# Performance work log

Measured on AMD Instinct MI355X. Metric: run time of the kernel, lower is better.

The kernel has to match this reference:

```python
import jax, jax.numpy as jnp
import numpy as np

B, S, D, H = 4, 2048, 768, 12


def setup_inputs() -> dict:
    key = jax.random.key(0)
    k1, k2, k3, k4 = jax.random.split(key, 4)
    std = D ** (-0.5)
    x = jax.random.normal(k1, (B, S, D), dtype=jnp.float32)
    W_QKV = jax.random.normal(k2, (3, D, D), dtype=jnp.float32) * std
    W_O = jax.random.normal(k3, (D, D), dtype=jnp.float32) * std
    token_positions = jnp.sort(jax.random.randint(k4, (B, S), 0, S), axis=-1).astype(jnp.int64)
    return {"x": x, "W_QKV": W_QKV, "W_O": W_O, "token_positions": token_positions,
            "num_heads": H, "theta": 10000}


def _apply_rope(t, cos, sin):
    # t: (B, H, S, Hd); cos/sin: (B, 1, S, Hd/2). Interleaved even/odd pairs.
    te, to = t[..., 0::2], t[..., 1::2]
    re = te * cos - to * sin
    ro = te * sin + to * cos
    return jnp.stack([re, ro], axis=-1).reshape(t.shape)


def reference(x, W_QKV, W_O, token_positions, num_heads, theta):
    b, s, d = x.shape
    hd = d // num_heads  # d_head = d_k = d_v
    # fused QKV projection: Q = x @ W_QKV[0].T etc.
    qkv = jnp.einsum('bsd,kod->kbso', x, W_QKV)              # (3, B, S, D)
    qkv = qkv.reshape(3, b, s, num_heads, hd).transpose(0, 1, 3, 2, 4)  # (3, B, H, S, Hd)
    q, k, v = qkv[0], qkv[1], qkv[2]
    # RoPE angles: pos * theta^(-2j/d_k)
    inv_freq = jnp.asarray(theta, x.dtype) ** (-(jnp.arange(0, hd, 2, dtype=x.dtype) / hd))
    angles = token_positions.astype(x.dtype)[..., None] * inv_freq    # (B, S, Hd/2)
    cos = jnp.cos(angles)[:, None]                                     # (B, 1, S, Hd/2)
    sin = jnp.sin(angles)[:, None]
    q = _apply_rope(q, cos, sin)
    k = _apply_rope(k, cos, sin)
    # causal attention
    scores = jnp.einsum('bhqd,bhkd->bhqk', q, k) / (hd ** 0.5)        # (B, H, S, S)
    causal = jnp.tril(jnp.ones((s, s), dtype=bool))
    scores = jnp.where(causal, scores, -jnp.inf)
    probs = jax.nn.softmax(scores, axis=-1)
    out = jnp.einsum('bhqk,bhkd->bhqd', probs, v)                      # (B, H, S, Hd)
    out = out.transpose(0, 2, 1, 3).reshape(b, s, d)
    return out @ W_O.T
```

## Files before the change

kernel.cpp:

```cpp
#include <hip/hip_runtime.h>
#include <hip/hip_bf16.h>

typedef __bf16 bf16;
typedef __bf16 bf16x8 __attribute__((ext_vector_type(8)));
typedef __bf16 bf16x4 __attribute__((ext_vector_type(4)));
typedef short  s16x4  __attribute__((ext_vector_type(4)));
typedef float  f32x4  __attribute__((ext_vector_type(4)));

#if defined(__has_builtin)
#if __has_builtin(__builtin_amdgcn_mfma_f32_16x16x16bf16_1k)
#define HAVE_MFMA16 1
#endif
#if __has_builtin(__builtin_amdgcn_exp2f)
#define EXP2(x) __builtin_amdgcn_exp2f(x)
#else
#define EXP2(x) exp2f(x)
#endif
#else
#define EXP2(x) exp2f(x)
#endif

__device__ __forceinline__ void gl_lds16(const void* g, void* l) {
  __builtin_amdgcn_global_load_lds(
      (__attribute__((address_space(1))) const void*)g,
      (__attribute__((address_space(3))) void*)l, 16, 0, 0);
}

__device__ __forceinline__ f32x4 mfma32(bf16x8 a, bf16x8 b, f32x4 c) {
  return __builtin_amdgcn_mfma_f32_16x16x32_bf16(a, b, c, 0, 0, 0);
}
#if HAVE_MFMA16
__device__ __forceinline__ f32x4 mfma16(s16x4 a, s16x4 b, f32x4 c) {
  return __builtin_amdgcn_mfma_f32_16x16x16bf16_1k(a, b, c, 0, 0, 0);
}
#endif

__global__ void prep(const float* __restrict__ a, bf16* __restrict__ da,
                     const float* __restrict__ b, bf16* __restrict__ db,
                     const float* __restrict__ c, bf16* __restrict__ dc,
                     const int* __restrict__ tpos, const int* __restrict__ thetap,
                     float2* __restrict__ tab) {
  int bx = blockIdx.x;
  if (bx >= 8448) {
    int i = (bx - 8448) * 256 + threadIdx.x;
    int d2 = i & 31;
    int bs = i >> 5;
    float lt = log2f((float)(*thetap));
    float fr = exp2f(-(float)d2 * (1.0f / 32.0f) * lt);
    float ang = (float)tpos[bs] * fr;
    float sn, cs;
    sincosf(ang, &sn, &cs);
    tab[i] = make_float2(cs, sn);
    return;
  }
  const float* s; bf16* d; int i;
  if (bx < 6144)      { s = a; d = da; i = bx * 256 + threadIdx.x; }
  else if (bx < 7872) { s = b; d = db; i = (bx - 6144) * 256 + threadIdx.x; }
  else                { s = c; d = dc; i = (bx - 7872) * 256 + threadIdx.x; }
  float4 v = ((const float4*)s)[i];
  bf16x4 o;
  o[0] = (bf16)v.x; o[1] = (bf16)v.y; o[2] = (bf16)v.z; o[3] = (bf16)v.w;
  ((bf16x4*)d)[i] = o;
}

template <int MODE>
__global__ void gemm_bt(const bf16* __restrict__ A, const bf16* __restrict__ Bm,
                        void* __restrict__ Cout, bf16* __restrict__ Vout,
                        const float2* __restrict__ tab) {
  constexpr int K = 768;
  __shared__ __align__(16) char As[2][128 * 64];
  __shared__ __align__(16) char Bs[2][128 * 64];
  const int tid = threadIdx.x;
  const int w = tid >> 6, lane = tid & 63;
  const int quad = lane >> 4, l15 = lane & 15;
  const int wrow = w >> 1, wcol = w & 1;
  const int m0 = blockIdx.x * 128, n0 = blockIdx.y * 128;

  f32x4 acc[4][4];
#pragma unroll
  for (int mt = 0; mt < 4; ++mt)
#pragma unroll
    for (int nt = 0; nt < 4; ++nt) acc[mt][nt] = (f32x4){0.f, 0.f, 0.f, 0.f};

  auto stage = [&](int k0, int bufi) {
#pragma unroll
    for (int i = 0; i < 2; ++i) {
      int L = i * 256 + tid;
      int r = L >> 2, cl = L & 3;
      int cg = cl ^ ((r >> 1) & 3);
      gl_lds16(A + (size_t)(m0 + r) * K + k0 + cg * 8, As[bufi] + (i * 256 + w * 64) * 16);
      gl_lds16(Bm + (size_t)(n0 + r) * K + k0 + cg * 8, Bs[bufi] + (i * 256 + w * 64) * 16);
    }
  };

  stage(0, 0);
  int buf = 0;

  for (int k0 = 0; k0 < K; k0 += 32) {
    __syncthreads();
    if (k0 + 32 < K) stage(k0 + 32, buf ^ 1);
    const char* Ab = As[buf];
    const char* Bb = Bs[buf];

    bf16x8 af[4], bfr[4];
#pragma unroll
    for (int mt = 0; mt < 4; ++mt) {
      int r = wrow * 64 + mt * 16 + l15;
      int cl = quad ^ ((r >> 1) & 3);
      af[mt] = *(const bf16x8*)(Ab + r * 64 + cl * 16);
    }
#pragma unroll
    for (int nt = 0; nt < 4; ++nt) {
      int r = wcol * 64 + nt * 16 + l15;
      int cl = quad ^ ((r >> 1) & 3);
      bfr[nt] = *(const bf16x8*)(Bb + r * 64 + cl * 16);
    }
#pragma unroll
    for (int mt = 0; mt < 4; ++mt)
#pragma unroll
      for (int nt = 0; nt < 4; ++nt)
        acc[mt][nt] = mfma32(af[mt], bfr[nt], acc[mt][nt]);
    buf ^= 1;
  }

#pragma unroll
  for (int mt = 0; mt < 4; ++mt)
#pragma unroll
    for (int nt = 0; nt < 4; ++nt)
#pragma unroll
      for (int r = 0; r < 4; ++r) {
        int m = m0 + wrow * 64 + mt * 16 + quad * 4 + r;
        int n = n0 + wcol * 64 + nt * 16 + l15;
        float v = acc[mt][nt][r];
        if (MODE == 0) {
          ((float*)Cout)[(size_t)m * 768 + n] = v;
        } else {
          int mat = n / 768, rem = n % 768;
          int hh = rem >> 6, d = rem & 63;
          int bb = m >> 11, s = m & 2047;
          if (mat == 2) {
            Vout[(((size_t)(bb * 12 + hh) * 64 + d) * 2048) + s] = (bf16)v;
          } else {
            float partner = __shfl_xor(v, 1);
            float2 t = tab[((size_t)m << 5) + ((rem >> 1) & 31)];
            float out = v * t.x + ((n & 1) ? partner : -partner) * t.y;
            if (mat == 0) out *= 0.18033688011112042f;
            ((bf16*)Cout)[(((size_t)(mat * 4 + bb) * 12 + hh) * 2048 + s) * 64 + d] = (bf16)out;
          }
        }
      }
}

__global__ __launch_bounds__(256, 4)
void attn(const bf16* __restrict__ qkv, const bf16* __restrict__ vt,
          bf16* __restrict__ aout) {
  const int bx = blockIdx.x;
  const int qt = 15 - (bx / 48);
  const int bh = bx % 48;
  const int b = bh / 12, h = bh % 12;
  const int tid = threadIdx.x, w = tid >> 6, lane = tid & 63;
  const int quad = lane >> 4, l15 = lane & 15;
  const bf16* Q  = qkv + (size_t)bh * (2048 * 64);
  const bf16* Kp = qkv + (size_t)(48 + bh) * (2048 * 64);
  const bf16* Vt = vt + (size_t)bh * (64 * 2048);
  __shared__ __align__(16) char Ks[2][64 * 128];
  __shared__ __align__(16) char Vs[2][64 * 128];

  const int qbase = qt * 128 + w * 32;
  const int kmax = qbase >> 6;
  bf16x8 qf[2][2];
#pragma unroll
  for (int j = 0; j < 2; ++j) {
    qf[j][0] = *(const bf16x8*)(Q + (size_t)(qbase + j * 16 + l15) * 64 + quad * 8);
    qf[j][1] = *(const bf16x8*)(Q + (size_t)(qbase + j * 16 + l15) * 64 + 32 + quad * 8);
  }

  float li[2] = {0.f, 0.f};
  f32x4 o[2][4];
#pragma unroll
  for (int j = 0; j < 2; ++j)
#pragma unroll
    for (int dt = 0; dt < 4; ++dt) o[j][dt] = (f32x4){0.f, 0.f, 0.f, 0.f};

  auto stage = [&](int kb, int bufi) {
#pragma unroll
    for (int i = 0; i < 2; ++i) {
      int L = i * 256 + tid;
      int r = L >> 3, cl = L & 7, cg = cl ^ (r & 7);
      gl_lds16(Kp + (size_t)(kb * 64 + r) * 64 + cg * 8, Ks[bufi] + L * 16);
      gl_lds16(Vt + (size_t)r * 2048 + kb * 64 + cg * 8, Vs[bufi] + L * 16);
    }
  };

  stage(0, 0);
  int buf = 0;
  const int nkt = 2 * qt + 2;

  for (int kb = 0; kb < nkt; ++kb) {
    __syncthreads();
    if (kb + 1 < nkt) stage(kb + 1, buf ^ 1);
    if (kb <= kmax) {
      const char* Kb = Ks[buf];
      const char* Vb = Vs[buf];

      float S[2][16];
      __builtin_amdgcn_s_setprio(1);
#pragma unroll
      for (int sk = 0; sk < 4; ++sk) {
        int r = sk * 16 + l15;
        int cl0 = quad ^ (r & 7);
        int cl1 = (4 + quad) ^ (r & 7);
        bf16x8 kf0 = *(const bf16x8*)(Kb + r * 128 + cl0 * 16);
        bf16x8 kf1 = *(const bf16x8*)(Kb + r * 128 + cl1 * 16);
#pragma unroll
        for (int j = 0; j < 2; ++j) {
          f32x4 st = (f32x4){0.f, 0.f, 0.f, 0.f};
          st = mfma32(kf0, qf[j][0], st);
          st = mfma32(kf1, qf[j][1], st);
#pragma unroll
          for (int rr = 0; rr < 4; ++rr) S[j][sk * 4 + rr] = st[rr];
        }
      }
      __builtin_amdgcn_s_setprio(0);
      if (kb == kmax) {
#pragma unroll
        for (int j = 0; j < 2; ++j)
#pragma unroll
          for (int sk = 0; sk < 4; ++sk)
#pragma unroll
            for (int rr = 0; rr < 4; ++rr) {
              int key = kb * 64 + sk * 16 + quad * 4 + rr;
              if (key > qbase + j * 16 + l15) S[j][sk * 4 + rr] = -1e30f;
            }
      }

#if HAVE_MFMA16
      s16x4 pf[2][4];
#endif
#pragma unroll
      for (int j = 0; j < 2; ++j) {
        float rs = 0.f;
#pragma unroll
        for (int sk = 0; sk < 4; ++sk) {
          bf16x4 pb;
#pragma unroll
          for (int rr = 0; rr < 4; ++rr) {
            float p = EXP2(S[j][sk * 4 + rr]);
            rs += p;
            pb[rr] = (bf16)p;
#if !HAVE_MFMA16
            S[j][sk * 4 + rr] = p;
#endif
          }
#if HAVE_MFMA16
          pf[j][sk] = __builtin_bit_cast(s16x4, pb);
#else
          (void)pb;
#endif
        }
        rs += __shfl_xor(rs, 16);
        rs += __shfl_xor(rs, 32);
        li[j] += rs;
      }

#if HAVE_MFMA16
      __builtin_amdgcn_s_setprio(1);
#pragma unroll
      for (int sk = 0; sk < 4; ++sk)
#pragma unroll
        for (int dt = 0; dt < 4; ++dt) {
          int rr = dt * 16 + l15;
          int c = sk * 2 + (quad >> 1);
          int cl = c ^ (rr & 7);
          s16x4 vf = *(const s16x4*)(Vb + rr * 128 + cl * 16 + (quad & 1) * 8);
          o[0][dt] = mfma16(pf[0][sk], vf, o[0][dt]);
          o[1][dt] = mfma16(pf[1][sk], vf, o[1][dt]);
        }
      __builtin_amdgcn_s_setprio(0);
#else
#pragma unroll
      for (int j = 0; j < 2; ++j)
#pragma unroll
        for (int kc = 0; kc < 2; ++kc) {
          bf16x8 af;
#pragma unroll
          for (int jj = 0; jj < 8; ++jj) {
            int sq = (quad & 1) * 2 + (jj >> 2);
            int src = sq * 16 + l15;
            float v0 = __shfl(S[j][kc * 8 + (jj & 3)], src);
            float v1 = __shfl(S[j][kc * 8 + 4 + (jj & 3)], src);
            af[jj] = (bf16)((quad < 2) ? v0 : v1);
          }
#pragma unroll
          for (int dt = 0; dt < 4; ++dt) {
            int rr = dt * 16 + l15;
            int c = kc * 4 + quad;
            int cl = c ^ (rr & 7);
            bf16x8 vf = *(const bf16x8*)(Vb + rr * 128 + cl * 16);
            o[j][dt] = mfma32(af, vf, o[j][dt]);
          }
        }
#endif
    }
    buf ^= 1;
  }

#pragma unroll
  for (int j = 0; j < 2; ++j) {
    float lr[4];
#pragma unroll
    for (int rr = 0; rr < 4; ++rr)
      lr[rr] = __builtin_amdgcn_rcpf(__shfl(li[j], quad * 4 + rr));
#pragma unroll
    for (int dt = 0; dt < 4; ++dt)
#pragma unroll
      for (int rr = 0; rr < 4; ++rr) {
        int q = qbase + j * 16 + quad * 4 + rr;
        int n = h * 64 + dt * 16 + l15;
        aout[((size_t)b * 2048 + q) * 768 + n] = (bf16)(o[j][dt][rr] * lr[rr]);
      }
  }
}

extern "C" void kernel_launch(void* const* d_in, const int* in_sizes, int n_in,
                              void* d_out, int out_size, void* d_ws, size_t ws_size,
                              hipStream_t stream) {
  const float* x    = (const float*)d_in[0];
  const float* wqkv = (const float*)d_in[1];
  const float* wo   = (const float*)d_in[2];
  const int* tpos   = (const int*)d_in[3];
  const int* thetap = (const int*)d_in[5];

  char* ws = (char*)d_ws;
  bf16* xb    = (bf16*)(ws);
  bf16* wqkvb = (bf16*)(ws + 12582912);
  bf16* wob   = (bf16*)(ws + 16121856);
  bf16* qkv   = (bf16*)(ws + 17301504);
  bf16* vtb   = (bf16*)(ws + 55050240);
  float2* tab = (float2*)(ws + 42467328);

  prep<<<9472, 256, 0, stream>>>(x, xb, wqkv, wqkvb, wo, wob, tpos, thetap, tab);
  gemm_bt<1><<<dim3(64, 18), 256, 0, stream>>>(xb, wqkvb, (void*)qkv, vtb, tab);
  attn<<<768, 256, 0, stream>>>(qkv, vtb, xb);
  gemm_bt<0><<<dim3(64, 6), 256, 0, stream>>>(xb, wob, (void*)d_out, nullptr, nullptr);
}
```

Baseline: 228.8 us.

## Shrink attention tiles, read V directly from global, add smaller-tile output GEMM

The attention kernel moves to 64-query tiles with 128 threads, doubling the block count. It stages only K through LDS and reads V fragments straight from global memory, dropping the V LDS buffer and the setprio hints. The output projection gets its own kernel with 64-row tiles and twice the blocks, so the CUs are better filled. In exchange, V global loads are not coalesced or cached in LDS, and the K/V reuse across queries within a block is halved.

```diff
diff --git a/kernel.cpp b/kernel.cpp
--- a/kernel.cpp
+++ b/kernel.cpp
@@ -63,10 +63,9 @@
   ((bf16x4*)d)[i] = o;
 }
 
-template <int MODE>
-__global__ void gemm_bt(const bf16* __restrict__ A, const bf16* __restrict__ Bm,
-                        void* __restrict__ Cout, bf16* __restrict__ Vout,
-                        const float2* __restrict__ tab) {
+__global__ void gemm_qkv(const bf16* __restrict__ A, const bf16* __restrict__ Bm,
+                         bf16* __restrict__ Cout, bf16* __restrict__ Vout,
+                         const float2* __restrict__ tab) {
   constexpr int K = 768;
   __shared__ __align__(16) char As[2][128 * 64];
   __shared__ __align__(16) char Bs[2][128 * 64];
@@ -132,30 +131,102 @@
         int m = m0 + wrow * 64 + mt * 16 + quad * 4 + r;
         int n = n0 + wcol * 64 + nt * 16 + l15;
         float v = acc[mt][nt][r];
-        if (MODE == 0) {
-          ((float*)Cout)[(size_t)m * 768 + n] = v;
+        int mat = n / 768, rem = n % 768;
+        int hh = rem >> 6, d = rem & 63;
+        int bb = m >> 11, s = m & 2047;
+        if (mat == 2) {
+          Vout[(((size_t)(bb * 12 + hh) * 64 + d) * 2048) + s] = (bf16)v;
         } else {
-          int mat = n / 768, rem = n % 768;
-          int hh = rem >> 6, d = rem & 63;
-          int bb = m >> 11, s = m & 2047;
-          if (mat == 2) {
-            Vout[(((size_t)(bb * 12 + hh) * 64 + d) * 2048) + s] = (bf16)v;
-          } else {
-            float partner = __shfl_xor(v, 1);
-            float2 t = tab[((size_t)m << 5) + ((rem >> 1) & 31)];
-            float out = v * t.x + ((n & 1) ? partner : -partner) * t.y;
-            if (mat == 0) out *= 0.18033688011112042f;
-            ((bf16*)Cout)[(((size_t)(mat * 4 + bb) * 12 + hh) * 2048 + s) * 64 + d] = (bf16)out;
-          }
+          float partner = __shfl_xor(v, 1);
+          float2 t = tab[((size_t)m << 5) + ((rem >> 1) & 31)];
+          float out = v * t.x + ((n & 1) ? partner : -partner) * t.y;
+          if (mat == 0) out *= 0.18033688011112042f;
+          Cout[(((size_t)(mat * 4 + bb) * 12 + hh) * 2048 + s) * 64 + d] = (bf16)out;
         }
       }
 }
 
 __global__ __launch_bounds__(256, 4)
+void gemm_o(const bf16* __restrict__ A, const bf16* __restrict__ Bm,
+            float* __restrict__ Cout) {
+  constexpr int K = 768;
+  __shared__ __align__(16) char As[2][64 * 64];
+  __shared__ __align__(16) char Bs[2][128 * 64];
+  const int tid = threadIdx.x;
+  const int w = tid >> 6, lane = tid & 63;
+  const int quad = lane >> 4, l15 = lane & 15;
+  const int wrow = w >> 1, wcol = w & 1;
+  const int m0 = blockIdx.x * 64, n0 = blockIdx.y * 128;
+
+  f32x4 acc[2][4];
+#pragma unroll
+  for (int mt = 0; mt < 2; ++mt)
+#pragma unroll
+    for (int nt = 0; nt < 4; ++nt) acc[mt][nt] = (f32x4){0.f, 0.f, 0.f, 0.f};
+
+  auto stage = [&](int k0, int bufi) {
+    {
+      int L = tid;
+      int r = L >> 2, cl = L & 3;
+      int cg = cl ^ ((r >> 1) & 3);
+      gl_lds16(A + (size_t)(m0 + r) * K + k0 + cg * 8, As[bufi] + (w * 64) * 16 + lane * 16);
+    }
+#pragma unroll
+    for (int i = 0; i < 2; ++i) {
+      int L = i * 256 + tid;
+      int r = L >> 2, cl = L & 3;
+      int cg = cl ^ ((r >> 1) & 3);
+      gl_lds16(Bm + (size_t)(n0 + r) * K + k0 + cg * 8, Bs[bufi] + (i * 256 + w * 64) * 16);
+    }
+  };
+
+  stage(0, 0);
+  int buf = 0;
+
+  for (int k0 = 0; k0 < K; k0 += 32) {
+    __syncthreads();
+    if (k0 + 32 < K) stage(k0 + 32, buf ^ 1);
+    const char* Ab = As[buf];
+    const char* Bb = Bs[buf];
+
+    bf16x8 af[2], bfr[4];
+#pragma unroll
+    for (int mt = 0; mt < 2; ++mt) {
+      int r = wrow * 32 + mt * 16 + l15;
+      int cl = quad ^ ((r >> 1) & 3);
+      af[mt] = *(const bf16x8*)(Ab + r * 64 + cl * 16);
+    }
+#pragma unroll
+    for (int nt = 0; nt < 4; ++nt) {
+      int r = wcol * 64 + nt * 16 + l15;
+      int cl = quad ^ ((r >> 1) & 3);
+      bfr[nt] = *(const bf16x8*)(Bb + r * 64 + cl * 16);
+    }
+#pragma unroll
+    for (int mt = 0; mt < 2; ++mt)
+#pragma unroll
+      for (int nt = 0; nt < 4; ++nt)
+        acc[mt][nt] = mfma32(af[mt], bfr[nt], acc[mt][nt]);
+    buf ^= 1;
+  }
+
+#pragma unroll
+  for (int mt = 0; mt < 2; ++mt)
+#pragma unroll
+    for (int nt = 0; nt < 4; ++nt)
+#pragma unroll
+      for (int r = 0; r < 4; ++r) {
+        int m = m0 + wrow * 32 + mt * 16 + quad * 4 + r;
+        int n = n0 + wcol * 64 + nt * 16 + l15;
+        Cout[(size_t)m * 768 + n] = acc[mt][nt][r];
+      }
+}
+
+__global__ __launch_bounds__(128, 5)
 void attn(const bf16* __restrict__ qkv, const bf16* __restrict__ vt,
           bf16* __restrict__ aout) {
   const int bx = blockIdx.x;
-  const int qt = 15 - (bx / 48);
+  const int qt = 31 - (bx / 48);
   const int bh = bx % 48;
   const int b = bh / 12, h = bh % 12;
   const int tid = threadIdx.x, w = tid >> 6, lane = tid & 63;
@@ -164,10 +235,8 @@
   const bf16* Kp = qkv + (size_t)(48 + bh) * (2048 * 64);
   const bf16* Vt = vt + (size_t)bh * (64 * 2048);
   __shared__ __align__(16) char Ks[2][64 * 128];
-  __shared__ __align__(16) char Vs[2][64 * 128];
-
-  const int qbase = qt * 128 + w * 32;
-  const int kmax = qbase >> 6;
+
+  const int qbase = qt * 64 + w * 32;
   bf16x8 qf[2][2];
 #pragma unroll
   for (int j = 0; j < 2; ++j) {
@@ -184,124 +253,113 @@
 
   auto stage = [&](int kb, int bufi) {
 #pragma unroll
-    for (int i = 0; i < 2; ++i) {
-      int L = i * 256 + tid;
+    for (int i = 0; i < 4; ++i) {
+      int L = i * 128 + tid;
       int r = L >> 3, cl = L & 7, cg = cl ^ (r & 7);
       gl_lds16(Kp + (size_t)(kb * 64 + r) * 64 + cg * 8, Ks[bufi] + L * 16);
-      gl_lds16(Vt + (size_t)r * 2048 + kb * 64 + cg * 8, Vs[bufi] + L * 16);
     }
   };
 
   stage(0, 0);
   int buf = 0;
-  const int nkt = 2 * qt + 2;
-
-  for (int kb = 0; kb < nkt; ++kb) {
+
+  for (int kb = 0; kb <= qt; ++kb) {
     __syncthreads();
-    if (kb + 1 < nkt) stage(kb + 1, buf ^ 1);
-    if (kb <= kmax) {
-      const char* Kb = Ks[buf];
-      const char* Vb = Vs[buf];
-
-      float S[2][16];
-      __builtin_amdgcn_s_setprio(1);
+    if (kb < qt) stage(kb + 1, buf ^ 1);
+    const char* Kb = Ks[buf];
+
+    float S[2][16];
+#pragma unroll
+    for (int sk = 0; sk < 4; ++sk) {
+      int r = sk * 16 + l15;
+      int cl0 = quad ^ (r & 7);
+      int cl1 = (4 + quad) ^ (r & 7);
+      bf16x8 kf0 = *(const bf16x8*)(Kb + r * 128 + cl0 * 16);
+      bf16x8 kf1 = *(const bf16x8*)(Kb + r * 128 + cl1 * 16);
+#pragma unroll
+      for (int j = 0; j < 2; ++j) {
+        f32x4 st = (f32x4){0.f, 0.f, 0.f, 0.f};
+        st = mfma32(kf0, qf[j][0], st);
+        st = mfma32(kf1, qf[j][1], st);
+#pragma unroll
+        for (int rr = 0; rr < 4; ++rr) S[j][sk * 4 + rr] = st[rr];
+      }
+    }
+    if (kb == qt) {
+#pragma unroll
+      for (int j = 0; j < 2; ++j)
+#pragma unroll
+        for (int sk = 0; sk < 4; ++sk)
+#pragma unroll
+          for (int rr = 0; rr < 4; ++rr) {
+            int key = kb * 64 + sk * 16 + quad * 4 + rr;
+            if (key > qbase + j * 16 + l15) S[j][sk * 4 + rr] = -1e30f;
+          }
+    }
+
+#if HAVE_MFMA16
+    s16x4 pf[2][4];
+#endif
+#pragma unroll
+    for (int j = 0; j < 2; ++j) {
+      float rs = 0.f;
 #pragma unroll
       for (int sk = 0; sk < 4; ++sk) {
-        int r = sk * 16 + l15;
-        int cl0 = quad ^ (r & 7);
-        int cl1 = (4 + quad) ^ (r & 7);
-        bf16x8 kf0 = *(const bf16x8*)(Kb + r * 128 + cl0 * 16);
-        bf16x8 kf1 = *(const bf16x8*)(Kb + r * 128 + cl1 * 16);
-#pragma unroll
-        for (int j = 0; j < 2; ++j) {
-          f32x4 st = (f32x4){0.f, 0.f, 0.f, 0.f};
-          st = mfma32(kf0, qf[j][0], st);
-          st = mfma32(kf1, qf[j][1], st);
-#pragma unroll
-          for (int rr = 0; rr < 4; ++rr) S[j][sk * 4 + rr] = st[rr];
+        bf16x4 pb;
+#pragma unroll
+        for (int rr = 0; rr < 4; ++rr) {
+          float p = EXP2(S[j][sk * 4 + rr]);
+          rs += p;
+          pb[rr] = (bf16)p;
+#if !HAVE_MFMA16
+          S[j][sk * 4 + rr] = p;
+#endif
         }
-      }
-      __builtin_amdgcn_s_setprio(0);
-      if (kb == kmax) {
-#pragma unroll
-        for (int j = 0; j < 2; ++j)
-#pragma unroll
-          for (int sk = 0; sk < 4; ++sk)
-#pragma unroll
-            for (int rr = 0; rr < 4; ++rr) {
-              int key = kb * 64 + sk * 16 + quad * 4 + rr;
-              if (key > qbase + j * 16 + l15) S[j][sk * 4 + rr] = -1e30f;
-            }
-      }
-
 #if HAVE_MFMA16
-      s16x4 pf[2][4];
-#endif
-#pragma unroll
-      for (int j = 0; j < 2; ++j) {
-        float rs = 0.f;
-#pragma unroll
-        for (int sk = 0; sk < 4; ++sk) {
-          bf16x4 pb;
-#pragma unroll
-          for (int rr = 0; rr < 4; ++rr) {
-            float p = EXP2(S[j][sk * 4 + rr]);
-            rs += p;
-            pb[rr] = (bf16)p;
-#if !HAVE_MFMA16
-            S[j][sk * 4 + rr] = p;
-#endif
-          }
+        pf[j][sk] = __builtin_bit_cast(s16x4, pb);
+#else
+        (void)pb;
+#endif
+      }
+      rs += __shfl_xor(rs, 16);
+      rs += __shfl_xor(rs, 32);
+      li[j] += rs;
+    }
+
 #if HAVE_MFMA16
-          pf[j][sk] = __builtin_bit_cast(s16x4, pb);
+#pragma unroll
+    for (int sk = 0; sk < 4; ++sk)
+#pragma unroll
+      for (int dt = 0; dt < 4; ++dt) {
+        int rr = dt * 16 + l15;
+        int c = sk * 2 + (quad >> 1);
+        s16x4 vf = *(const s16x4*)(Vt + (size_t)rr * 2048 + kb * 64 + c * 8 + (quad & 1) * 4);
+        o[0][dt] = mfma16(pf[0][sk], vf, o[0][dt]);
+        o[1][dt] = mfma16(pf[1][sk], vf, o[1][dt]);
+      }
 #else
-          (void)pb;
-#endif
+#pragma unroll
+    for (int j = 0; j < 2; ++j)
+#pragma unroll
+      for (int kc = 0; kc < 2; ++kc) {
+        bf16x8 af;
+#pragma unroll
+        for (int jj = 0; jj < 8; ++jj) {
+          int sq = (quad & 1) * 2 + (jj >> 2);
+          int src = sq * 16 + l15;
+          float v0 = __shfl(S[j][kc * 8 + (jj & 3)], src);
+          float v1 = __shfl(S[j][kc * 8 + 4 + (jj & 3)], src);
+          af[jj] = (bf16)((quad < 2) ? v0 : v1);
         }
-        rs += __shfl_xor(rs, 16);
-        rs += __shfl_xor(rs, 32);
-        li[j] += rs;
-      }
-
-#if HAVE_MFMA16
-      __builtin_amdgcn_s_setprio(1);
-#pragma unroll
-      for (int sk = 0; sk < 4; ++sk)
 #pragma unroll
         for (int dt = 0; dt < 4; ++dt) {
           int rr = dt * 16 + l15;
-          int c = sk * 2 + (quad >> 1);
-          int cl = c ^ (rr & 7);
-          s16x4 vf = *(const s16x4*)(Vb + rr * 128 + cl * 16 + (quad & 1) * 8);
-          o[0][dt] = mfma16(pf[0][sk], vf, o[0][dt]);
-          o[1][dt] = mfma16(pf[1][sk], vf, o[1][dt]);
+          int c = kc * 4 + quad;
+          bf16x8 vf = *(const bf16x8*)(Vt + (size_t)rr * 2048 + kb * 64 + c * 8);
+          o[j][dt] = mfma32(af, vf, o[j][dt]);
         }
-      __builtin_amdgcn_s_setprio(0);
-#else
-#pragma unroll
-      for (int j = 0; j < 2; ++j)
-#pragma unroll
-        for (int kc = 0; kc < 2; ++kc) {
-          bf16x8 af;
-#pragma unroll
-          for (int jj = 0; jj < 8; ++jj) {
-            int sq = (quad & 1) * 2 + (jj >> 2);
-            int src = sq * 16 + l15;
-            float v0 = __shfl(S[j][kc * 8 + (jj & 3)], src);
-            float v1 = __shfl(S[j][kc * 8 + 4 + (jj & 3)], src);
-            af[jj] = (bf16)((quad < 2) ? v0 : v1);
-          }
-#pragma unroll
-          for (int dt = 0; dt < 4; ++dt) {
-            int rr = dt * 16 + l15;
-            int c = kc * 4 + quad;
-            int cl = c ^ (rr & 7);
-            bf16x8 vf = *(const bf16x8*)(Vb + rr * 128 + cl * 16);
-            o[j][dt] = mfma32(af, vf, o[j][dt]);
-          }
-        }
-#endif
-    }
+      }
+#endif
     buf ^= 1;
   }
 
@@ -340,7 +398,7 @@
   float2* tab = (float2*)(ws + 42467328);
 
   prep<<<9472, 256, 0, stream>>>(x, xb, wqkv, wqkvb, wo, wob, tpos, thetap, tab);
-  gemm_bt<1><<<dim3(64, 18), 256, 0, stream>>>(xb, wqkvb, (void*)qkv, vtb, tab);
-  attn<<<768, 256, 0, stream>>>(qkv, vtb, xb);
-  gemm_bt<0><<<dim3(64, 6), 256, 0, stream>>>(xb, wob, (void*)d_out, nullptr, nullptr);
-}
+  gemm_qkv<<<dim3(64, 18), 256, 0, stream>>>(xb, wqkvb, qkv, vtb, tab);
+  attn<<<1536, 128, 0, stream>>>(qkv, vtb, xb);
+  gemm_o<<<dim3(128, 6), 256, 0, stream>>>(xb, wob, (float*)d_out);
+}
```

After: 383.7 us. 67.7% more time.
